# Optimization experiments

Measured on AMD Instinct MI355X. Metric: run time of the kernel, lower is better.

## Reference

```python
import jax, jax.numpy as jnp
import numpy as np

MARGIN = 0.3


def _l2norm(x, axis=-1):
    return x / (jnp.linalg.norm(x, axis=axis, keepdims=True) + 1e-12)


def setup_inputs() -> dict:
    key = jax.random.key(0)
    k1, k2, k3, k4 = jax.random.split(key, 4)
    n, P, d = 1024, 8, 2048
    global_feat = jax.random.normal(k1, (n, d), dtype=jnp.float32)
    partial_feat = jax.random.normal(k2, (n, P, d), dtype=jnp.float32)
    part_labels = jax.random.randint(k3, (n, P), 0, 2).astype(jnp.float32)
    global_labels = jax.random.randint(k4, (n,), 0, 64).astype(jnp.int64)
    return {"global_feat": global_feat, "partial_feat": partial_feat,
            "part_labels": part_labels, "global_labels": global_labels}


def reference(global_feat, partial_feat, part_labels, global_labels):
    # --- compute_distance (VGTripletLoss) ---
    g = _l2norm(global_feat)            # [n, d]
    p = _l2norm(partial_feat)           # [n, P, d]
    gs = (1.0 - g @ g.T) / 2.0          # [n, n]
    overlap = part_labels[:, None, :] * part_labels[None, :, :]   # [n, n, P]
    # per-part cosine distance: [n, n, P]
    slf = (1.0 - jnp.einsum('ipd,jpd->ijp', p, p)) / 2.0
    slf = slf * overlap
    dist = (slf.sum(-1) + gs) / (overlap.sum(-1) + 1.0)            # [n, n]

    # --- compute_loss: hard positive/negative mining ---
    mask = global_labels[:, None] == global_labels[None, :]        # [n, n]
    neg_inf = jnp.float32(-1e30)
    pos_inf = jnp.float32(1e30)
    dist_ap = jnp.max(jnp.where(mask, dist, neg_inf), axis=1)      # hardest positive
    dist_an = jnp.min(jnp.where(mask, pos_inf, dist), axis=1)      # hardest negative
    # MarginRankingLoss(y=1, reduction='mean'): max(0, dist_ap - dist_an + margin)
    loss = jnp.mean(jax.nn.relu(dist_ap - dist_an + MARGIN))
    return loss
```

## Files before the change

### kernel.cpp

```cpp
#include <hip/hip_runtime.h>

#define N 1024
#define D 2048
#define P 8
#define F 9
#define KTOT (F * D)
#define SPLIT 8
#define KS (KTOT / SPLIT)
#define BM 128
#define BKT 32
#define MARGIN 0.3f

typedef float f32x4 __attribute__((ext_vector_type(4)));
typedef short s16x8 __attribute__((ext_vector_type(8)));

#define GLOBAL_AS __attribute__((address_space(1)))
#define LDS_AS __attribute__((address_space(3)))

__device__ __forceinline__ const float* feat_row(const float* __restrict__ g,
                                                 const float* __restrict__ p,
                                                 int i, int f) {
    return (f == 0) ? (g + (size_t)i * D)
                    : (p + ((size_t)i * P + (f - 1)) * D);
}

__device__ __forceinline__ unsigned f2bf(float x) {
    unsigned u = __float_as_uint(x);
    return (u + 0x7fffu + ((u >> 16) & 1u)) >> 16;
}

__global__ void pack_kernel(const float* __restrict__ gfeat,
                            const float* __restrict__ pfeat,
                            const float* __restrict__ plab,
                            unsigned short* __restrict__ V) {
    const int r = blockIdx.x;
    const int i = r / F, f = r % F;
    const float* src = feat_row(gfeat, pfeat, i, f);
    const int t = threadIdx.x;
    const float4* s4 = (const float4*)src;
    float4 a = s4[2 * t];
    float4 b = s4[2 * t + 1];
    float ss = a.x*a.x + a.y*a.y + a.z*a.z + a.w*a.w
             + b.x*b.x + b.y*b.y + b.z*b.z + b.w*b.w;
    __shared__ float red[256];
    __shared__ float invs;
    red[t] = ss;
    __syncthreads();
    for (int s = 128; s > 0; s >>= 1) {
        if (t < s) red[t] += red[t + s];
        __syncthreads();
    }
    if (t == 0) {
        float ls = (f == 0) ? 1.0f : plab[i * P + (f - 1)];
        invs = ls / (sqrtf(red[0]) + 1e-12f);
    }
    __syncthreads();
    const float inv = invs;
    uint4 o;
    o.x = f2bf(a.x * inv) | (f2bf(a.y * inv) << 16);
    o.y = f2bf(a.z * inv) | (f2bf(a.w * inv) << 16);
    o.z = f2bf(b.x * inv) | (f2bf(b.y * inv) << 16);
    o.w = f2bf(b.z * inv) | (f2bf(b.w * inv) << 16);
    *(uint4*)&V[(size_t)r * D + t * 8] = o;
}

__global__ __launch_bounds__(256)
void gemm_kernel(const unsigned short* __restrict__ V,
                 float* __restrict__ part) {
    __shared__ short As[BM * BKT];
    __shared__ short Bs[BM * BKT];

    const int t = threadIdx.x;
    const int wave = t >> 6, lane = t & 63;
    const int i0 = blockIdx.y * BM;
    const int j0 = blockIdx.x * BM;
    const int kbase = blockIdx.z * KS;

    const unsigned short* Ap = V + (size_t)(i0 + (t >> 2)) * KTOT + kbase + (t & 3) * 8;
    const unsigned short* Bp = V + (size_t)(j0 + (t >> 2)) * KTOT + kbase + (t & 3) * 8;

    const int kq = lane >> 4;
    const short* Abase = As + ((wave & 1) * 64 + (lane & 15)) * BKT + kq * 8;
    const short* Bbase = Bs + ((wave >> 1) * 64 + (lane & 15)) * BKT + kq * 8;

    f32x4 acc[4][4];
    #pragma unroll
    for (int m = 0; m < 4; ++m)
        #pragma unroll
        for (int n = 0; n < 4; ++n)
            acc[m][n] = (f32x4){0.f, 0.f, 0.f, 0.f};

    for (int ks = 0; ks < KS / BKT; ++ks) {
        __syncthreads();
        __builtin_amdgcn_global_load_lds((const GLOBAL_AS void*)Ap,
                                         (LDS_AS void*)(As + t * 8), 16, 0, 0);
        __builtin_amdgcn_global_load_lds((const GLOBAL_AS void*)(Ap + (size_t)64 * KTOT),
                                         (LDS_AS void*)(As + 2048 + t * 8), 16, 0, 0);
        __builtin_amdgcn_global_load_lds((const GLOBAL_AS void*)Bp,
                                         (LDS_AS void*)(Bs + t * 8), 16, 0, 0);
        __builtin_amdgcn_global_load_lds((const GLOBAL_AS void*)(Bp + (size_t)64 * KTOT),
                                         (LDS_AS void*)(Bs + 2048 + t * 8), 16, 0, 0);
        Ap += BKT;
        Bp += BKT;
        __syncthreads();

        s16x8 af[4], bf[4];
        #pragma unroll
        for (int m = 0; m < 4; ++m) af[m] = *(const s16x8*)(Abase + m * 16 * BKT);
        #pragma unroll
        for (int n = 0; n < 4; ++n) bf[n] = *(const s16x8*)(Bbase + n * 16 * BKT);
        #pragma unroll
        for (int m = 0; m < 4; ++m)
            #pragma unroll
            for (int n = 0; n < 4; ++n)
                acc[m][n] = __builtin_amdgcn_mfma_f32_16x16x32_bf16(
                    af[m], bf[n], acc[m][n], 0, 0, 0);
    }

    float* outp = part + (size_t)blockIdx.z * N * N;
    const int rbase = i0 + (wave & 1) * 64 + (lane >> 4) * 4;
    const int cbase = j0 + (wave >> 1) * 64 + (lane & 15);
    #pragma unroll
    for (int m = 0; m < 4; ++m)
        #pragma unroll
        for (int n = 0; n < 4; ++n)
            #pragma unroll
            for (int r = 0; r < 4; ++r)
                outp[(size_t)(rbase + m * 16 + r) * N + cbase + n * 16] = acc[m][n][r];
}

__global__ void mine_kernel(const float* __restrict__ part,
                            const float* __restrict__ plab,
                            const int* __restrict__ glab,
                            float* __restrict__ rowloss) {
    const int i = blockIdx.x;
    const int t = threadIdx.x;
    const int li = glab[i];
    float lab_i[P];
    #pragma unroll
    for (int c = 0; c < P; ++c) lab_i[c] = plab[i * P + c];

    float ap = -1e30f, an = 1e30f;
    for (int j = t; j < N; j += 256) {
        float dot = 0.f;
        #pragma unroll
        for (int s = 0; s < SPLIT; ++s)
            dot += part[(size_t)s * N * N + (size_t)i * N + j];
        float ov = 0.f;
        #pragma unroll
        for (int c = 0; c < P; ++c) ov += lab_i[c] * plab[j * P + c];
        float d = 0.5f - dot / (2.0f * (ov + 1.0f));
        if (glab[j] == li) ap = fmaxf(ap, d);
        else               an = fminf(an, d);
    }
    __shared__ float smax[256], smin[256];
    smax[t] = ap; smin[t] = an;
    __syncthreads();
    for (int s = 128; s > 0; s >>= 1) {
        if (t < s) {
            smax[t] = fmaxf(smax[t], smax[t + s]);
            smin[t] = fminf(smin[t], smin[t + s]);
        }
        __syncthreads();
    }
    if (t == 0) rowloss[i] = fmaxf(0.f, smax[0] - smin[0] + MARGIN);
}

__global__ void reduce_kernel(const float* __restrict__ rowloss,
                              float* __restrict__ out) {
    const int t = threadIdx.x;
    float s = rowloss[t] + rowloss[t + 256] + rowloss[t + 512] + rowloss[t + 768];
    __shared__ float red[256];
    red[t] = s;
    __syncthreads();
    for (int st = 128; st > 0; st >>= 1) {
        if (t < st) red[t] += red[t + st];
        __syncthreads();
    }
    if (t == 0) out[0] = red[0] * (1.0f / N);
}

extern "C" void kernel_launch(void* const* d_in, const int* in_sizes, int n_in,
                              void* d_out, int out_size, void* d_ws, size_t ws_size,
                              hipStream_t stream) {
    const float* gfeat = (const float*)d_in[0];
    const float* pfeat = (const float*)d_in[1];
    const float* plab  = (const float*)d_in[2];
    const int*   glab  = (const int*)d_in[3];
    float* out = (float*)d_out;

    char* ws = (char*)d_ws;
    unsigned short* V = (unsigned short*)ws;
    float* part    = (float*)(ws + (size_t)37748736);
    float* rowloss = (float*)(ws + (size_t)37748736 + 33554432);

    pack_kernel<<<N * F, 256, 0, stream>>>(gfeat, pfeat, plab, V);
    gemm_kernel<<<dim3(N / BM, N / BM, SPLIT), 256, 0, stream>>>(V, part);
    mine_kernel<<<N, 256, 0, stream>>>(part, plab, glab, rowloss);
    reduce_kernel<<<1, 256, 0, stream>>>(rowloss, out);
}
```

Measured before the change: 171.6 us.

## Raise split-K with atomic slot accumulation, swizzle LDS, wave-per-row pack, fuse reduce

Split-K goes from 8 to 16 so the GEMM grid has twice as many blocks. Partial products are accumulated with atomics into 8 zeroed slots, which keeps the mining read size unchanged. The LDS tile layout gets an XOR swizzle to reduce bank conflicts. The pack kernel now uses one wave per row with a shuffle reduction instead of a block-wide shared-memory reduction. The final reduce kernel is removed by having each mining block atomically add its scaled row loss into the output. The cost is two memsets, atomic-add traffic in the GEMM epilogue, and an order-dependent floating-point sum.

```diff
diff --git a/kernel.cpp b/kernel.cpp
--- a/kernel.cpp
+++ b/kernel.cpp
@@ -5,7 +5,8 @@
 #define P 8
 #define F 9
 #define KTOT (F * D)
-#define SPLIT 8
+#define SPLIT 16
+#define NSLOT 8
 #define KS (KTOT / SPLIT)
 #define BM 128
 #define BKT 32
@@ -29,42 +30,36 @@
     return (u + 0x7fffu + ((u >> 16) & 1u)) >> 16;
 }
 
-__global__ void pack_kernel(const float* __restrict__ gfeat,
-                            const float* __restrict__ pfeat,
-                            const float* __restrict__ plab,
-                            unsigned short* __restrict__ V) {
-    const int r = blockIdx.x;
+__global__ __launch_bounds__(256)
+void pack_kernel(const float* __restrict__ gfeat,
+                 const float* __restrict__ pfeat,
+                 const float* __restrict__ plab,
+                 unsigned short* __restrict__ V) {
+    const int wave = threadIdx.x >> 6, lane = threadIdx.x & 63;
+    const int r = blockIdx.x * 4 + wave;
     const int i = r / F, f = r % F;
-    const float* src = feat_row(gfeat, pfeat, i, f);
-    const int t = threadIdx.x;
-    const float4* s4 = (const float4*)src;
-    float4 a = s4[2 * t];
-    float4 b = s4[2 * t + 1];
-    float ss = a.x*a.x + a.y*a.y + a.z*a.z + a.w*a.w
-             + b.x*b.x + b.y*b.y + b.z*b.z + b.w*b.w;
-    __shared__ float red[256];
-    __shared__ float invs;
-    red[t] = ss;
-    __syncthreads();
-    for (int s = 128; s > 0; s >>= 1) {
-        if (t < s) red[t] += red[t + s];
-        __syncthreads();
+    const float4* s4 = (const float4*)feat_row(gfeat, pfeat, i, f);
+    float4 v[8];
+    float ss = 0.f;
+    #pragma unroll
+    for (int q = 0; q < 8; ++q) {
+        v[q] = s4[lane + 64 * q];
+        ss += v[q].x*v[q].x + v[q].y*v[q].y + v[q].z*v[q].z + v[q].w*v[q].w;
     }
-    if (t == 0) {
-        float ls = (f == 0) ? 1.0f : plab[i * P + (f - 1)];
-        invs = ls / (sqrtf(red[0]) + 1e-12f);
+    #pragma unroll
+    for (int m = 32; m >= 1; m >>= 1) ss += __shfl_xor(ss, m, 64);
+    const float ls = (f == 0) ? 1.0f : plab[i * P + (f - 1)];
+    const float inv = ls / (sqrtf(ss) + 1e-12f);
+    #pragma unroll
+    for (int q = 0; q < 8; ++q) {
+        uint2 o;
+        o.x = f2bf(v[q].x * inv) | (f2bf(v[q].y * inv) << 16);
+        o.y = f2bf(v[q].z * inv) | (f2bf(v[q].w * inv) << 16);
+        *(uint2*)&V[(size_t)r * D + (lane + 64 * q) * 4] = o;
     }
-    __syncthreads();
-    const float inv = invs;
-    uint4 o;
-    o.x = f2bf(a.x * inv) | (f2bf(a.y * inv) << 16);
-    o.y = f2bf(a.z * inv) | (f2bf(a.w * inv) << 16);
-    o.z = f2bf(b.x * inv) | (f2bf(b.y * inv) << 16);
-    o.w = f2bf(b.z * inv) | (f2bf(b.w * inv) << 16);
-    *(uint4*)&V[(size_t)r * D + t * 8] = o;
 }
 
-__global__ __launch_bounds__(256)
+__global__ __launch_bounds__(256, 4)
 void gemm_kernel(const unsigned short* __restrict__ V,
                  float* __restrict__ part) {
     __shared__ short As[BM * BKT];
@@ -76,12 +71,16 @@
     const int j0 = blockIdx.x * BM;
     const int kbase = blockIdx.z * KS;
 
-    const unsigned short* Ap = V + (size_t)(i0 + (t >> 2)) * KTOT + kbase + (t & 3) * 8;
-    const unsigned short* Bp = V + (size_t)(j0 + (t >> 2)) * KTOT + kbase + (t & 3) * 8;
+    const int srow = t >> 2;
+    const int schunk = (t & 3) ^ (srow & 3);
+    const unsigned short* Ap = V + (size_t)(i0 + srow) * KTOT + kbase + schunk * 8;
+    const unsigned short* Bp = V + (size_t)(j0 + srow) * KTOT + kbase + schunk * 8;
 
     const int kq = lane >> 4;
-    const short* Abase = As + ((wave & 1) * 64 + (lane & 15)) * BKT + kq * 8;
-    const short* Bbase = Bs + ((wave >> 1) * 64 + (lane & 15)) * BKT + kq * 8;
+    const int rA = (wave & 1) * 64 + (lane & 15);
+    const int rB = (wave >> 1) * 64 + (lane & 15);
+    const short* Abase = As + rA * BKT + (kq ^ (rA & 3)) * 8;
+    const short* Bbase = Bs + rB * BKT + (kq ^ (rB & 3)) * 8;
 
     f32x4 acc[4][4];
     #pragma unroll
@@ -117,7 +116,7 @@
                     af[m], bf[n], acc[m][n], 0, 0, 0);
     }
 
-    float* outp = part + (size_t)blockIdx.z * N * N;
+    float* outp = part + (size_t)(blockIdx.z & (NSLOT - 1)) * N * N;
     const int rbase = i0 + (wave & 1) * 64 + (lane >> 4) * 4;
     const int cbase = j0 + (wave >> 1) * 64 + (lane & 15);
     #pragma unroll
@@ -126,13 +125,14 @@
         for (int n = 0; n < 4; ++n)
             #pragma unroll
             for (int r = 0; r < 4; ++r)
-                outp[(size_t)(rbase + m * 16 + r) * N + cbase + n * 16] = acc[m][n][r];
+                unsafeAtomicAdd(&outp[(size_t)(rbase + m * 16 + r) * N + cbase + n * 16],
+                                acc[m][n][r]);
 }
 
 __global__ void mine_kernel(const float* __restrict__ part,
                             const float* __restrict__ plab,
                             const int* __restrict__ glab,
-                            float* __restrict__ rowloss) {
+                            float* __restrict__ out) {
     const int i = blockIdx.x;
     const int t = threadIdx.x;
     const int li = glab[i];
@@ -144,7 +144,7 @@
     for (int j = t; j < N; j += 256) {
         float dot = 0.f;
         #pragma unroll
-        for (int s = 0; s < SPLIT; ++s)
+        for (int s = 0; s < NSLOT; ++s)
             dot += part[(size_t)s * N * N + (size_t)i * N + j];
         float ov = 0.f;
         #pragma unroll
@@ -163,21 +163,10 @@
         }
         __syncthreads();
     }
-    if (t == 0) rowloss[i] = fmaxf(0.f, smax[0] - smin[0] + MARGIN);
-}
-
-__global__ void reduce_kernel(const float* __restrict__ rowloss,
-                              float* __restrict__ out) {
-    const int t = threadIdx.x;
-    float s = rowloss[t] + rowloss[t + 256] + rowloss[t + 512] + rowloss[t + 768];
-    __shared__ float red[256];
-    red[t] = s;
-    __syncthreads();
-    for (int st = 128; st > 0; st >>= 1) {
-        if (t < st) red[t] += red[t + st];
-        __syncthreads();
+    if (t == 0) {
+        float loss = fmaxf(0.f, smax[0] - smin[0] + MARGIN);
+        unsafeAtomicAdd(out, loss * (1.0f / N));
     }
-    if (t == 0) out[0] = red[0] * (1.0f / N);
 }
 
 extern "C" void kernel_launch(void* const* d_in, const int* in_sizes, int n_in,
@@ -191,11 +180,11 @@
 
     char* ws = (char*)d_ws;
     unsigned short* V = (unsigned short*)ws;
-    float* part    = (float*)(ws + (size_t)37748736);
-    float* rowloss = (float*)(ws + (size_t)37748736 + 33554432);
+    float* part = (float*)(ws + (size_t)37748736);
 
-    pack_kernel<<<N * F, 256, 0, stream>>>(gfeat, pfeat, plab, V);
+    hipMemsetAsync(part, 0, (size_t)NSLOT * N * N * sizeof(float), stream);
+    hipMemsetAsync(out, 0, sizeof(float), stream);
+    pack_kernel<<<(N * F) / 4, 256, 0, stream>>>(gfeat, pfeat, plab, V);
     gemm_kernel<<<dim3(N / BM, N / BM, SPLIT), 256, 0, stream>>>(V, part);
-    mine_kernel<<<N, 256, 0, stream>>>(part, plab, glab, rowloss);
-    reduce_kernel<<<1, 256, 0, stream>>>(rowloss, out);
+    mine_kernel<<<N, 256, 0, stream>>>(part, plab, glab, out);
 }
```

Measured after the change: 221.2 us. 28.9% more time.
